# Kernel tuning notes

Hardware: AMD Instinct MI355X
Metric: run time of the kernel (lower is better)

## Reference

```python
import jax, jax.numpy as jnp
import numpy as np

N, E = 50000, 800000
IN_D, HID, H1, OUT_D, H2, EDGE_D = 64, 16, 8, 64, 2, 1
NEG_SLOPE = 0.2


def gatv2_layer(x, src, dst, edge_attr, Wl, Wr, We, att, bias, concat):
    """PyG GATv2Conv (add_self_loops=False, share_weights=False), eval mode (no dropout)."""
    n = x.shape[0]
    H, C = att.shape
    xl = (x @ Wl).reshape(n, H, C)            # source transform
    xr = (x @ Wr).reshape(n, H, C)            # target transform
    ee = (edge_attr @ We).reshape(-1, H, C)   # edge embedding
    z = jax.nn.leaky_relu(xl[src] + xr[dst] + ee, NEG_SLOPE)  # [E,H,C]
    score = jnp.einsum('ehc,hc->eh', z, att)                  # [E,H]
    # softmax over incoming edges per target node
    m = jax.ops.segment_max(score, dst, num_segments=n)
    m = jnp.where(jnp.isfinite(m), m, 0.0)
    a = jnp.exp(score - m[dst])
    denom = jax.ops.segment_sum(a, dst, num_segments=n)
    alpha = a / (denom[dst] + 1e-16)                          # [E,H]
    msg = xl[src] * alpha[..., None]                          # [E,H,C]
    out = jax.ops.segment_sum(msg, dst, num_segments=n)       # [N,H,C]
    if concat:
        return out.reshape(n, H * C) + bias
    return out.mean(axis=1) + bias


def layer_norm(x, g, b):
    mu = x.mean(-1, keepdims=True)
    var = ((x - mu) ** 2).mean(-1, keepdims=True)
    return (x - mu) * jax.lax.rsqrt(var + 1e-5) * g + b


def setup_inputs() -> dict:
    key = jax.random.key(0)
    ks = jax.random.split(key, 24)
    def w(k, *shape):
        fan_in = shape[0]
        return jax.random.normal(k, shape, dtype=jnp.float32) * (1.0 / np.sqrt(fan_in))
    inp = {
        'x': jax.random.normal(ks[0], (N, IN_D), dtype=jnp.float32),
        'edge_index': jax.random.randint(ks[1], (2, E), 0, N, dtype=jnp.int64),
        'edge_attr': jax.random.normal(ks[2], (E, EDGE_D), dtype=jnp.float32),
        # layer 1 (heads=8, out=16, concat)
        'w1_l': w(ks[3], IN_D, H1 * HID), 'w1_r': w(ks[4], IN_D, H1 * HID),
        'w1_e': w(ks[5], EDGE_D, H1 * HID),
        'att1': jax.random.normal(ks[6], (H1, HID), dtype=jnp.float32) * 0.1,
        'b1': jnp.zeros((H1 * HID,), dtype=jnp.float32),
        # layer 2 (heads=2, out=64, mean)
        'w2_l': w(ks[7], H1 * HID, H2 * OUT_D), 'w2_r': w(ks[8], H1 * HID, H2 * OUT_D),
        'w2_e': w(ks[9], EDGE_D, H2 * OUT_D),
        'att2': jax.random.normal(ks[10], (H2, OUT_D), dtype=jnp.float32) * 0.1,
        'b2': jnp.zeros((OUT_D,), dtype=jnp.float32),
        # classifier: Linear + LayerNorm + GELU + ResidualBlockv2
        'wc': w(ks[11], OUT_D, OUT_D), 'bc': jnp.zeros((OUT_D,), dtype=jnp.float32),
        'ln_g': jnp.ones((OUT_D,), dtype=jnp.float32), 'ln_b': jnp.zeros((OUT_D,), dtype=jnp.float32),
        'wr': w(ks[12], OUT_D, OUT_D), 'br': jnp.zeros((OUT_D,), dtype=jnp.float32),
        'lnr_g': jnp.ones((OUT_D,), dtype=jnp.float32), 'lnr_b': jnp.zeros((OUT_D,), dtype=jnp.float32),
    }
    return inp


def reference(x, edge_index, edge_attr, w1_l, w1_r, w1_e, att1, b1,
              w2_l, w2_r, w2_e, att2, b2, wc, bc, ln_g, ln_b, wr, br, lnr_g, lnr_b):
    src, dst = edge_index[0], edge_index[1]
    h = jax.nn.relu(gatv2_layer(x, src, dst, edge_attr, w1_l, w1_r, w1_e, att1, b1, True))
    h = jax.nn.relu(gatv2_layer(h, src, dst, edge_attr, w2_l, w2_r, w2_e, att2, b2, False))
    h = jax.nn.gelu(layer_norm(h @ wc + bc, ln_g, ln_b), approximate=False)
    # ResidualBlockv2: Linear -> LayerNorm -> GELU with residual skip
    h = h + jax.nn.gelu(layer_norm(h @ wr + br, lnr_g, lnr_b), approximate=False)
    return h
```

## Files before the change

### kernel.cpp

```cpp
#include <hip/hip_runtime.h>
#include <math.h>

#define NNODE 50000
#define NEDGE 800000
#define NBLK_SCAN 196

__device__ __forceinline__ float wsum64(float v) {
    #pragma unroll
    for (int m = 32; m >= 1; m >>= 1) v += __shfl_xor(v, m, 64);
    return v;
}

__device__ __forceinline__ float gelu_exact(float x) {
    return 0.5f * x * (1.0f + erff(x * 0.70710678118654752f));
}

__device__ __forceinline__ float lrelu(float z) { return z > 0.f ? z : 0.2f * z; }

__global__ void fill_u32(unsigned* __restrict__ p, unsigned v, int n) {
    int i = blockIdx.x * blockDim.x + threadIdx.x;
    if (i < n) p[i] = v;
}

__global__ __launch_bounds__(256) void build_deg(const int* __restrict__ ei, int* __restrict__ deg) {
    int e = blockIdx.x * 256 + threadIdx.x;
    if (e >= NEDGE) return;
    atomicAdd(&deg[ei[NEDGE + e]], 1);
}

__global__ __launch_bounds__(256) void scan1(const int* __restrict__ deg,
                                             int* __restrict__ partial,
                                             int* __restrict__ bsum) {
    __shared__ int tmp[256];
    int t = threadIdx.x;
    int gid = blockIdx.x * 256 + t;
    int v = (gid < NNODE) ? deg[gid] : 0;
    tmp[t] = v;
    __syncthreads();
    #pragma unroll
    for (int off = 1; off < 256; off <<= 1) {
        int u = (t >= off) ? tmp[t - off] : 0;
        __syncthreads();
        tmp[t] += u;
        __syncthreads();
    }
    if (gid < NNODE) partial[gid] = tmp[t] - v;
    if (t == 255) bsum[blockIdx.x] = tmp[255];
}

__global__ __launch_bounds__(256) void scan2(int* __restrict__ bsum, int* __restrict__ boff) {
    __shared__ int tmp[256];
    int t = threadIdx.x;
    int v = (t < NBLK_SCAN) ? bsum[t] : 0;
    tmp[t] = v;
    __syncthreads();
    #pragma unroll
    for (int off = 1; off < 256; off <<= 1) {
        int u = (t >= off) ? tmp[t - off] : 0;
        __syncthreads();
        tmp[t] += u;
        __syncthreads();
    }
    if (t < NBLK_SCAN) boff[t] = tmp[t] - v;
}

__global__ __launch_bounds__(256) void scan3(const int* __restrict__ partial,
                                             const int* __restrict__ boff,
                                             int* __restrict__ base,
                                             int* __restrict__ cursor) {
    int gid = blockIdx.x * 256 + threadIdx.x;
    if (gid < NNODE) {
        int b = partial[gid] + boff[blockIdx.x];
        base[gid] = b;
        cursor[gid] = b;
    }
    if (gid == 0) base[NNODE] = NEDGE;
}

__global__ __launch_bounds__(256) void scatter_edges(const int* __restrict__ ei,
                                                     const float* __restrict__ ea,
                                                     int* __restrict__ cursor,
                                                     int2* __restrict__ se) {
    int e = blockIdx.x * 256 + threadIdx.x;
    if (e >= NEDGE) return;
    int d = ei[NEDGE + e];
    int i = atomicAdd(&cursor[d], 1);
    se[i] = make_int2(ei[e], __float_as_int(ea[e]));
}

__global__ __launch_bounds__(256) void node_xform1(const float* __restrict__ x,
                                                   const float* __restrict__ wl,
                                                   const float* __restrict__ wr,
                                                   float* __restrict__ xl,
                                                   float* __restrict__ xr) {
    __shared__ float xrow[8][64];
    int t = threadIdx.x;
    int n0 = blockIdx.x * 8;
    for (int k = t; k < 8 * 64; k += 256) xrow[k >> 6][k & 63] = x[(size_t)n0 * 64 + k];
    __syncthreads();
    const float* w;
    float* o;
    int c;
    if (t < 128) { w = wl; c = t; o = xl; }
    else         { w = wr; c = t - 128; o = xr; }
    float acc[8] = {0.f, 0.f, 0.f, 0.f, 0.f, 0.f, 0.f, 0.f};
    for (int i = 0; i < 64; ++i) {
        float wv = w[i * 128 + c];
        #pragma unroll
        for (int k = 0; k < 8; ++k) acc[k] += xrow[k][i] * wv;
    }
    #pragma unroll
    for (int k = 0; k < 8; ++k) o[(size_t)(n0 + k) * 128 + c] = acc[k];
}

__global__ __launch_bounds__(256) void node_xform2(const float* __restrict__ h1,
                                                   const float* __restrict__ wl,
                                                   const float* __restrict__ wr,
                                                   float* __restrict__ xl,
                                                   float* __restrict__ xr) {
    __shared__ float hrow[8][128];
    int t = threadIdx.x;
    int n0 = blockIdx.x * 8;
    for (int k = t; k < 8 * 128; k += 256) hrow[k >> 7][k & 127] = h1[(size_t)n0 * 128 + k];
    __syncthreads();
    const float* w;
    float* o;
    int c;
    if (t < 128) { w = wl; c = t; o = xl; }
    else         { w = wr; c = t - 128; o = xr; }
    float acc[8] = {0.f, 0.f, 0.f, 0.f, 0.f, 0.f, 0.f, 0.f};
    for (int i = 0; i < 128; ++i) {
        float wv = w[i * 128 + c];
        #pragma unroll
        for (int k = 0; k < 8; ++k) acc[k] += hrow[k][i] * wv;
    }
    #pragma unroll
    for (int k = 0; k < 8; ++k) o[(size_t)(n0 + k) * 128 + c] = acc[k];
}

__global__ __launch_bounds__(256) void fused1(const int* __restrict__ base,
                                              const int2* __restrict__ se,
                                              const float* __restrict__ xl,
                                              const float* __restrict__ xr,
                                              const float* __restrict__ w1e,
                                              const float* __restrict__ att1,
                                              const float* __restrict__ b1,
                                              float* __restrict__ h1) {
    int t = threadIdx.x;
    int wv = t >> 6, ln = t & 63;
    int half = ln >> 5, sub = ln & 31;
    int n = blockIdx.x * 4 + wv;
    int ch = sub * 4;
    float4 xrv = *(const float4*)(xr + (size_t)n * 128 + ch);
    float4 wev = *(const float4*)(w1e + ch);
    float4 atv = *(const float4*)(att1 + ch);
    int i0 = base[n], i1 = base[n + 1];
    float m = -1e30f, den = 0.f;
    float4 o = make_float4(0.f, 0.f, 0.f, 0.f);
    int i = i0 + half;
    if (i < i1) {
        int2 r = se[i];
        float4 xv = *(const float4*)(xl + (size_t)r.x * 128 + ch);
        float a = __int_as_float(r.y);
        for (i += 2; i < i1; i += 2) {
            int2 rn = se[i];
            float4 nxv = *(const float4*)(xl + (size_t)rn.x * 128 + ch);
            float na = __int_as_float(rn.y);
            float part = lrelu(fmaf(a, wev.x, xv.x + xrv.x)) * atv.x
                       + lrelu(fmaf(a, wev.y, xv.y + xrv.y)) * atv.y
                       + lrelu(fmaf(a, wev.z, xv.z + xrv.z)) * atv.z
                       + lrelu(fmaf(a, wev.w, xv.w + xrv.w)) * atv.w;
            part += __shfl_xor(part, 1, 64);
            part += __shfl_xor(part, 2, 64);
            float mn = fmaxf(m, part);
            float sc = __expf(m - mn);
            float p  = __expf(part - mn);
            den = den * sc + p;
            o.x = o.x * sc + p * xv.x;
            o.y = o.y * sc + p * xv.y;
            o.z = o.z * sc + p * xv.z;
            o.w = o.w * sc + p * xv.w;
            m = mn;
            xv = nxv; a = na;
        }
        float part = lrelu(fmaf(a, wev.x, xv.x + xrv.x)) * atv.x
                   + lrelu(fmaf(a, wev.y, xv.y + xrv.y)) * atv.y
                   + lrelu(fmaf(a, wev.z, xv.z + xrv.z)) * atv.z
                   + lrelu(fmaf(a, wev.w, xv.w + xrv.w)) * atv.w;
        part += __shfl_xor(part, 1, 64);
        part += __shfl_xor(part, 2, 64);
        float mn = fmaxf(m, part);
        float sc = __expf(m - mn);
        float p  = __expf(part - mn);
        den = den * sc + p;
        o.x = o.x * sc + p * xv.x;
        o.y = o.y * sc + p * xv.y;
        o.z = o.z * sc + p * xv.z;
        o.w = o.w * sc + p * xv.w;
        m = mn;
    }
    float m2   = __shfl_xor(m, 32, 64);
    float den2 = __shfl_xor(den, 32, 64);
    float4 o2;
    o2.x = __shfl_xor(o.x, 32, 64);
    o2.y = __shfl_xor(o.y, 32, 64);
    o2.z = __shfl_xor(o.z, 32, 64);
    o2.w = __shfl_xor(o.w, 32, 64);
    float mn = fmaxf(m, m2);
    float s1 = __expf(m - mn), s2 = __expf(m2 - mn);
    den = den * s1 + den2 * s2;
    float inv = 1.f / (den + 1e-16f);
    if (half == 0) {
        float4 bv = *(const float4*)(b1 + ch);
        float4 res;
        res.x = fmaxf((o.x * s1 + o2.x * s2) * inv + bv.x, 0.f);
        res.y = fmaxf((o.y * s1 + o2.y * s2) * inv + bv.y, 0.f);
        res.z = fmaxf((o.z * s1 + o2.z * s2) * inv + bv.z, 0.f);
        res.w = fmaxf((o.w * s1 + o2.w * s2) * inv + bv.w, 0.f);
        *(float4*)(h1 + (size_t)n * 128 + ch) = res;
    }
}

__global__ __launch_bounds__(256) void fused2(const int* __restrict__ base,
                                              const int2* __restrict__ se,
                                              const float* __restrict__ xl,
                                              const float* __restrict__ xr,
                                              const float* __restrict__ w2e,
                                              const float* __restrict__ att2,
                                              const float* __restrict__ b2,
                                              float* __restrict__ h2) {
    int t = threadIdx.x;
    int wv = t >> 6, ln = t & 63;
    int half = ln >> 5, sub = ln & 31;
    int n = blockIdx.x * 4 + wv;
    int ch = sub * 4;
    float4 xrv = *(const float4*)(xr + (size_t)n * 128 + ch);
    float4 wev = *(const float4*)(w2e + ch);
    float4 atv = *(const float4*)(att2 + ch);
    int i0 = base[n], i1 = base[n + 1];
    float m = -1e30f, den = 0.f;
    float4 o = make_float4(0.f, 0.f, 0.f, 0.f);
    int i = i0 + half;
    if (i < i1) {
        int2 r = se[i];
        float4 xv = *(const float4*)(xl + (size_t)r.x * 128 + ch);
        float a = __int_as_float(r.y);
        for (i += 2; i < i1; i += 2) {
            int2 rn = se[i];
            float4 nxv = *(const float4*)(xl + (size_t)rn.x * 128 + ch);
            float na = __int_as_float(rn.y);
            float part = lrelu(fmaf(a, wev.x, xv.x + xrv.x)) * atv.x
                       + lrelu(fmaf(a, wev.y, xv.y + xrv.y)) * atv.y
                       + lrelu(fmaf(a, wev.z, xv.z + xrv.z)) * atv.z
                       + lrelu(fmaf(a, wev.w, xv.w + xrv.w)) * atv.w;
            part += __shfl_xor(part, 1, 64);
            part += __shfl_xor(part, 2, 64);
            part += __shfl_xor(part, 4, 64);
            part += __shfl_xor(part, 8, 64);
            float mn = fmaxf(m, part);
            float sc = __expf(m - mn);
            float p  = __expf(part - mn);
            den = den * sc + p;
            o.x = o.x * sc + p * xv.x;
            o.y = o.y * sc + p * xv.y;
            o.z = o.z * sc + p * xv.z;
            o.w = o.w * sc + p * xv.w;
            m = mn;
            xv = nxv; a = na;
        }
        float part = lrelu(fmaf(a, wev.x, xv.x + xrv.x)) * atv.x
                   + lrelu(fmaf(a, wev.y, xv.y + xrv.y)) * atv.y
                   + lrelu(fmaf(a, wev.z, xv.z + xrv.z)) * atv.z
                   + lrelu(fmaf(a, wev.w, xv.w + xrv.w)) * atv.w;
        part += __shfl_xor(part, 1, 64);
        part += __shfl_xor(part, 2, 64);
        part += __shfl_xor(part, 4, 64);
        part += __shfl_xor(part, 8, 64);
        float mn = fmaxf(m, part);
        float sc = __expf(m - mn);
        float p  = __expf(part - mn);
        den = den * sc + p;
        o.x = o.x * sc + p * xv.x;
        o.y = o.y * sc + p * xv.y;
        o.z = o.z * sc + p * xv.z;
        o.w = o.w * sc + p * xv.w;
        m = mn;
    }
    float m2   = __shfl_xor(m, 32, 64);
    float den2 = __shfl_xor(den, 32, 64);
    float4 o2;
    o2.x = __shfl_xor(o.x, 32, 64);
    o2.y = __shfl_xor(o.y, 32, 64);
    o2.z = __shfl_xor(o.z, 32, 64);
    o2.w = __shfl_xor(o.w, 32, 64);
    float mn = fmaxf(m, m2);
    float s1 = __expf(m - mn), s2 = __expf(m2 - mn);
    den = den * s1 + den2 * s2;
    float inv = 1.f / (den + 1e-16f);
    float4 v;
    v.x = (o.x * s1 + o2.x * s2) * inv;
    v.y = (o.y * s1 + o2.y * s2) * inv;
    v.z = (o.z * s1 + o2.z * s2) * inv;
    v.w = (o.w * s1 + o2.w * s2) * inv;
    float4 u;
    u.x = __shfl_xor(v.x, 16, 64);
    u.y = __shfl_xor(v.y, 16, 64);
    u.z = __shfl_xor(v.z, 16, 64);
    u.w = __shfl_xor(v.w, 16, 64);
    if (half == 0 && sub < 16) {
        float4 bv = *(const float4*)(b2 + ch);
        float4 res;
        res.x = fmaxf(0.5f * (v.x + u.x) + bv.x, 0.f);
        res.y = fmaxf(0.5f * (v.y + u.y) + bv.y, 0.f);
        res.z = fmaxf(0.5f * (v.z + u.z) + bv.z, 0.f);
        res.w = fmaxf(0.5f * (v.w + u.w) + bv.w, 0.f);
        *(float4*)(h2 + (size_t)n * 64 + ch) = res;
    }
}

__global__ __launch_bounds__(256) void classifier(const float* __restrict__ h2,
                                                  const float* __restrict__ wc,
                                                  const float* __restrict__ bc,
                                                  const float* __restrict__ lng,
                                                  const float* __restrict__ lnb,
                                                  const float* __restrict__ wr,
                                                  const float* __restrict__ br,
                                                  const float* __restrict__ lrg,
                                                  const float* __restrict__ lrb,
                                                  float* __restrict__ out) {
    __shared__ float rowA[4][64];
    __shared__ float rowB[4][64];
    int t = threadIdx.x;
    int wv = t >> 6, ln = t & 63;
    int n = blockIdx.x * 4 + wv;
    rowA[wv][ln] = h2[(size_t)n * 64 + ln];
    __syncthreads();
    float acc = bc[ln];
    #pragma unroll 8
    for (int i = 0; i < 64; ++i) acc += rowA[wv][i] * wc[i * 64 + ln];
    float mu = wsum64(acc) * (1.f / 64.f);
    float dv = acc - mu;
    float var = wsum64(dv * dv) * (1.f / 64.f);
    float y = dv * rsqrtf(var + 1e-5f) * lng[ln] + lnb[ln];
    float g1 = gelu_exact(y);
    rowB[wv][ln] = g1;
    __syncthreads();
    float acc2 = br[ln];
    #pragma unroll 8
    for (int i = 0; i < 64; ++i) acc2 += rowB[wv][i] * wr[i * 64 + ln];
    float mu2 = wsum64(acc2) * (1.f / 64.f);
    float dv2 = acc2 - mu2;
    float var2 = wsum64(dv2 * dv2) * (1.f / 64.f);
    float y2 = dv2 * rsqrtf(var2 + 1e-5f) * lrg[ln] + lrb[ln];
    float g2 = gelu_exact(y2);
    out[(size_t)n * 64 + ln] = g1 + g2;
}

extern "C" void kernel_launch(void* const* d_in, const int* in_sizes, int n_in,
                              void* d_out, int out_size, void* d_ws, size_t ws_size,
                              hipStream_t stream) {
    const float* x    = (const float*)d_in[0];
    const int*   ei   = (const int*)d_in[1];
    const float* ea   = (const float*)d_in[2];
    const float* w1l  = (const float*)d_in[3];
    const float* w1r  = (const float*)d_in[4];
    const float* w1e  = (const float*)d_in[5];
    const float* att1 = (const float*)d_in[6];
    const float* b1   = (const float*)d_in[7];
    const float* w2l  = (const float*)d_in[8];
    const float* w2r  = (const float*)d_in[9];
    const float* w2e  = (const float*)d_in[10];
    const float* att2 = (const float*)d_in[11];
    const float* b2   = (const float*)d_in[12];
    const float* wc   = (const float*)d_in[13];
    const float* bc   = (const float*)d_in[14];
    const float* lng  = (const float*)d_in[15];
    const float* lnb  = (const float*)d_in[16];
    const float* wr   = (const float*)d_in[17];
    const float* br   = (const float*)d_in[18];
    const float* lrg  = (const float*)d_in[19];
    const float* lrb  = (const float*)d_in[20];

    float* ws = (float*)d_ws;
    const size_t N128 = (size_t)NNODE * 128;
    float* xl = ws;
    float* xr = xl + N128;
    float* h1 = xr + N128;
    float* h2 = h1 + N128;
    int2*  se      = (int2*)(h2 + (size_t)NNODE * 64);
    int*   deg     = (int*)(se + NEDGE);
    int*   partial = deg + NNODE;
    int*   base    = partial + NNODE;
    int*   cursor  = base + NNODE + 1;
    int*   bsum    = cursor + NNODE;
    int*   boff    = bsum + 256;

    const int EB = NEDGE / 256;
    const int NB8 = NNODE / 8;
    const int NB4 = NNODE / 4;

    fill_u32<<<NBLK_SCAN, 256, 0, stream>>>((unsigned*)deg, 0u, NNODE);
    build_deg<<<EB, 256, 0, stream>>>(ei, deg);
    scan1<<<NBLK_SCAN, 256, 0, stream>>>(deg, partial, bsum);
    scan2<<<1, 256, 0, stream>>>(bsum, boff);
    scan3<<<NBLK_SCAN, 256, 0, stream>>>(partial, boff, base, cursor);
    scatter_edges<<<EB, 256, 0, stream>>>(ei, ea, cursor, se);

    node_xform1<<<NB8, 256, 0, stream>>>(x, w1l, w1r, xl, xr);
    fused1<<<NB4, 256, 0, stream>>>(base, se, xl, xr, w1e, att1, b1, h1);

    node_xform2<<<NB8, 256, 0, stream>>>(h1, w2l, w2r, xl, xr);
    fused2<<<NB4, 256, 0, stream>>>(base, se, xl, xr, w2e, att2, b2, h2);

    classifier<<<NB4, 256, 0, stream>>>(h2, wc, bc, lng, lnb, wr, br, lrg, lrb,
                                        (float*)d_out);
}
```

Measured before the change: 373.3 us.

## Register-tile node transforms: 32 nodes per block, float4 columns and weights

Merges the two node-transform kernels into one template and re-tiles it. Each block now handles 32 nodes, and each thread computes 8 nodes by 4 output columns with float4 loads of weights and staged inputs. The aim is more reuse of each weight load and fewer global and shared-memory transactions per FMA in these dense GEMMs. The cost is higher register pressure, plus bounds checks for the partial last tile.

New measurement: 351.6 us. 5.8% less time.

```diff
diff --git a/kernel.cpp b/kernel.cpp
--- a/kernel.cpp
+++ b/kernel.cpp
@@ -88,54 +88,50 @@
     se[i] = make_int2(ei[e], __float_as_int(ea[e]));
 }
 
-__global__ __launch_bounds__(256) void node_xform1(const float* __restrict__ x,
-                                                   const float* __restrict__ wl,
-                                                   const float* __restrict__ wr,
-                                                   float* __restrict__ xl,
-                                                   float* __restrict__ xr) {
-    __shared__ float xrow[8][64];
-    int t = threadIdx.x;
-    int n0 = blockIdx.x * 8;
-    for (int k = t; k < 8 * 64; k += 256) xrow[k >> 6][k & 63] = x[(size_t)n0 * 64 + k];
+template<int K>
+__global__ __launch_bounds__(256) void node_xform(const float* __restrict__ in,
+                                                  const float* __restrict__ wl,
+                                                  const float* __restrict__ wr,
+                                                  float* __restrict__ xl,
+                                                  float* __restrict__ xr) {
+    __shared__ float xrow[32][K];
+    int t = threadIdx.x;
+    int n0 = blockIdx.x * 32;
+    for (int idx = t; idx < 32 * (K / 4); idx += 256) {
+        int row = idx / (K / 4), c4 = idx % (K / 4);
+        float4 v = make_float4(0.f, 0.f, 0.f, 0.f);
+        if (n0 + row < NNODE) v = ((const float4*)(in + (size_t)(n0 + row) * K))[c4];
+        ((float4*)xrow[row])[c4] = v;
+    }
     __syncthreads();
-    const float* w;
-    float* o;
-    int c;
-    if (t < 128) { w = wl; c = t; o = xl; }
-    else         { w = wr; c = t - 128; o = xr; }
-    float acc[8] = {0.f, 0.f, 0.f, 0.f, 0.f, 0.f, 0.f, 0.f};
-    for (int i = 0; i < 64; ++i) {
-        float wv = w[i * 128 + c];
+    int cg = t & 63, ns = t >> 6;
+    const float* wsel = (cg < 32) ? wl : wr;
+    float* osel = (cg < 32) ? xl : xr;
+    int ccol = (cg & 31) * 4;
+    const float* wp = wsel + ccol;
+    const float* xbase = xrow[ns * 8];
+    float4 acc[8];
+    #pragma unroll
+    for (int k = 0; k < 8; ++k) acc[k] = make_float4(0.f, 0.f, 0.f, 0.f);
+    for (int i = 0; i < K; i += 4) {
+        float4 w0 = *(const float4*)(wp + (size_t)(i + 0) * 128);
+        float4 w1 = *(const float4*)(wp + (size_t)(i + 1) * 128);
+        float4 w2 = *(const float4*)(wp + (size_t)(i + 2) * 128);
+        float4 w3 = *(const float4*)(wp + (size_t)(i + 3) * 128);
         #pragma unroll
-        for (int k = 0; k < 8; ++k) acc[k] += xrow[k][i] * wv;
+        for (int k = 0; k < 8; ++k) {
+            float4 xv = *(const float4*)(xbase + (size_t)k * K + i);
+            acc[k].x += xv.x * w0.x + xv.y * w1.x + xv.z * w2.x + xv.w * w3.x;
+            acc[k].y += xv.x * w0.y + xv.y * w1.y + xv.z * w2.y + xv.w * w3.y;
+            acc[k].z += xv.x * w0.z + xv.y * w1.z + xv.z * w2.z + xv.w * w3.z;
+            acc[k].w += xv.x * w0.w + xv.y * w1.w + xv.z * w2.w + xv.w * w3.w;
+        }
     }
     #pragma unroll
-    for (int k = 0; k < 8; ++k) o[(size_t)(n0 + k) * 128 + c] = acc[k];
-}
-
-__global__ __launch_bounds__(256) void node_xform2(const float* __restrict__ h1,
-                                                   const float* __restrict__ wl,
-                                                   const float* __restrict__ wr,
-                                                   float* __restrict__ xl,
-                                                   float* __restrict__ xr) {
-    __shared__ float hrow[8][128];
-    int t = threadIdx.x;
-    int n0 = blockIdx.x * 8;
-    for (int k = t; k < 8 * 128; k += 256) hrow[k >> 7][k & 127] = h1[(size_t)n0 * 128 + k];
-    __syncthreads();
-    const float* w;
-    float* o;
-    int c;
-    if (t < 128) { w = wl; c = t; o = xl; }
-    else         { w = wr; c = t - 128; o = xr; }
-    float acc[8] = {0.f, 0.f, 0.f, 0.f, 0.f, 0.f, 0.f, 0.f};
-    for (int i = 0; i < 128; ++i) {
-        float wv = w[i * 128 + c];
-        #pragma unroll
-        for (int k = 0; k < 8; ++k) acc[k] += hrow[k][i] * wv;
-    }
-    #pragma unroll
-    for (int k = 0; k < 8; ++k) o[(size_t)(n0 + k) * 128 + c] = acc[k];
+    for (int k = 0; k < 8; ++k) {
+        int n = n0 + ns * 8 + k;
+        if (n < NNODE) *(float4*)(osel + (size_t)n * 128 + ccol) = acc[k];
+    }
 }
 
 __global__ __launch_bounds__(256) void fused1(const int* __restrict__ base,
@@ -395,8 +391,8 @@
     int*   bsum    = cursor + NNODE;
     int*   boff    = bsum + 256;
 
-    const int EB = NEDGE / 256;
-    const int NB8 = NNODE / 8;
+    const int EB  = NEDGE / 256;
+    const int NBX = (NNODE + 31) / 32;
     const int NB4 = NNODE / 4;
 
     fill_u32<<<NBLK_SCAN, 256, 0, stream>>>((unsigned*)deg, 0u, NNODE);
@@ -406,10 +402,10 @@
     scan3<<<NBLK_SCAN, 256, 0, stream>>>(partial, boff, base, cursor);
     scatter_edges<<<EB, 256, 0, stream>>>(ei, ea, cursor, se);
 
-    node_xform1<<<NB8, 256, 0, stream>>>(x, w1l, w1r, xl, xr);
+    node_xform<64><<<NBX, 256, 0, stream>>>(x, w1l, w1r, xl, xr);
     fused1<<<NB4, 256, 0, stream>>>(base, se, xl, xr, w1e, att1, b1, h1);
 
-    node_xform2<<<NB8, 256, 0, stream>>>(h1, w2l, w2r, xl, xr);
+    node_xform<128><<<NBX, 256, 0, stream>>>(h1, w2l, w2r, xl, xr);
     fused2<<<NB4, 256, 0, stream>>>(base, se, xl, xr, w2e, att2, b2, h2);
 
     classifier<<<NB4, 256, 0, stream>>>(h2, wc, bc, lng, lnb, wr, br, lrg, lrb,
```
